# Optimization experiments

Hardware: AMD Instinct MI355X
Metric: run time of the kernel (lower is better)

## Reference

```python
import jax, jax.numpy as jnp
import numpy as np

B, L, D = 64, 1024, 1024


def _attn(q, K, V, mask):
    # q: [B,D], K/V: [B,L,D], mask: [B,L] bool (True = valid)
    scores = jnp.einsum('bd,bld->bl', q, K) / jnp.sqrt(jnp.asarray(D, q.dtype))
    scores = jnp.where(mask, scores, -jnp.inf)
    attn = jax.nn.softmax(scores, axis=-1)
    attn = jnp.where(jnp.isnan(attn), 0.0, attn)  # torch.nan_to_num for all-masked rows
    return jnp.einsum('bl,bld->bd', attn, V)


def setup_inputs() -> dict:
    key = jax.random.key(0)
    ks = jax.random.split(key, 12)
    xav = float(np.sqrt(6.0 / (D + D)))  # xavier_uniform for square Linear
    img_mask = jax.random.randint(ks[4], (B, L), 0, 2).astype(bool)
    txt_mask = jax.random.randint(ks[7], (B, L), 0, 2).astype(bool)
    # guarantee at least one valid token per row
    img_mask = img_mask.at[:, 0].set(True)
    txt_mask = txt_mask.at[:, 0].set(True)
    return {
        'img_q': jax.random.normal(ks[0], (B, D), jnp.float32),
        'txt_q': jax.random.normal(ks[1], (B, D), jnp.float32),
        'K_img': jax.random.normal(ks[2], (B, L, D), jnp.float32),
        'V_img': jax.random.normal(ks[3], (B, L, D), jnp.float32),
        'img_mask': img_mask,
        'K_txt': jax.random.normal(ks[5], (B, L, D), jnp.float32),
        'V_txt': jax.random.normal(ks[6], (B, L, D), jnp.float32),
        'txt_mask': txt_mask,
        'W_img': jax.random.uniform(ks[8], (D, D), jnp.float32, -xav, xav),
        'b_img': jnp.zeros((D,), jnp.float32),
        'W_txt': jax.random.uniform(ks[9], (D, D), jnp.float32, -xav, xav),
        'b_txt': jnp.zeros((D,), jnp.float32),
    }


def reference(img_q, txt_q, K_img, V_img, img_mask, K_txt, V_txt, txt_mask,
              W_img, b_img, W_txt, b_txt):
    # Dropout is identity in eval mode.
    ctx_img = _attn(txt_q, K_img, V_img, img_mask)
    img_q = img_q + ctx_img @ W_img.T + b_img
    ctx_txt = _attn(img_q, K_txt, V_txt, txt_mask)
    txt_q = txt_q + ctx_txt @ W_txt.T + b_txt
    return (img_q, txt_q)
```

## Files before the change

### kernel.cpp

```cpp
#include <hip/hip_runtime.h>
#include <hip/hip_bf16.h>
#include <float.h>

#define B_ 64
#define L_ 1024
#define D_ 1024
#define NSPLIT 8
#define CHUNK 128
#define PSTRIDE 1028

typedef __bf16 bf16x8 __attribute__((ext_vector_type(8)));
typedef float f32x4 __attribute__((ext_vector_type(4)));

__device__ inline unsigned short f2bf(float x) {
    unsigned int u = __float_as_uint(x);
    unsigned int lsb = (u >> 16) & 1u;
    u += 0x7fffu + lsb;
    return (unsigned short)(u >> 16);
}

__global__ __launch_bounds__(512, 2) void attn_kernel(
    const float* __restrict__ q,
    const float* __restrict__ K,
    const float* __restrict__ V,
    const int*   __restrict__ mask,
    float* __restrict__ part,
    const float* __restrict__ cs0,
    const float* __restrict__ cs1,
    unsigned short* __restrict__ cd0,
    unsigned short* __restrict__ cd1,
    int nattn)
{
    const int tid = threadIdx.x;

    if ((int)blockIdx.x >= nattn) {
        int i = ((int)blockIdx.x - nattn) * 512 + tid;
        float4 v0 = reinterpret_cast<const float4*>(cs0)[i];
        float4 v1 = reinterpret_cast<const float4*>(cs1)[i];
        ushort4 u0, u1;
        u0.x = f2bf(v0.x); u0.y = f2bf(v0.y); u0.z = f2bf(v0.z); u0.w = f2bf(v0.w);
        u1.x = f2bf(v1.x); u1.y = f2bf(v1.y); u1.z = f2bf(v1.z); u1.w = f2bf(v1.w);
        reinterpret_cast<ushort4*>(cd0)[i] = u0;
        reinterpret_cast<ushort4*>(cd1)[i] = u1;
        return;
    }

    const int bid  = blockIdx.x;
    const int b    = bid >> 3;
    const int sp   = bid & 7;
    const int l0   = sp * CHUNK;
    const int wave = tid >> 6;
    const int lane = tid & 63;

    __shared__ int   vidx[CHUNK];
    __shared__ float sc[CHUNK];
    __shared__ float pw[CHUNK];
    __shared__ int   nvalid;

    const float4* qptr = reinterpret_cast<const float4*>(q + (size_t)b * D_);
    float4 qreg[4];
    #pragma unroll
    for (int rep = 0; rep < 4; ++rep) qreg[rep] = qptr[lane + rep * 64];

    if (wave == 0) {
        const int* mp = mask + (size_t)b * L_ + l0;
        int mv0 = mp[lane];
        int mv1 = mp[64 + lane];
        unsigned long long bal0 = __ballot(mv0 != 0);
        unsigned long long bal1 = __ballot(mv1 != 0);
        int n0 = __popcll(bal0);
        int nv = n0 + __popcll(bal1);
        unsigned long long lt = (1ull << lane) - 1;
        if (mv0) vidx[__popcll(bal0 & lt)] = lane;
        if (mv1) vidx[n0 + __popcll(bal1 & lt)] = 64 + lane;
        int padv = bal0 ? (__ffsll((long long)bal0) - 1)
                        : (bal1 ? 64 + __ffsll((long long)bal1) - 1 : 0);
        if (nv + lane < CHUNK) vidx[nv + lane] = padv;
        if (lane == 0) nvalid = nv;
    }
    __syncthreads();
    const int nv    = nvalid;
    const int nvp8  = (nv + 7)  & ~7;
    const int nvp16 = (nv + 15) & ~15;

    const float* Kb = K + ((size_t)b * L_ + l0) * D_;
    for (int jj = wave; jj < nvp16; jj += 16) {
        int j2 = jj + 8;
        const float4* k0 = reinterpret_cast<const float4*>(Kb + vidx[jj] * D_);
        const float4* k1 = reinterpret_cast<const float4*>(Kb + vidx[j2] * D_);
        float4 kv0[4], kv1[4];
        #pragma unroll
        for (int rep = 0; rep < 4; ++rep) { kv0[rep] = k0[lane + rep * 64];
                                            kv1[rep] = k1[lane + rep * 64]; }
        float a0a = 0.f, a0b = 0.f, a1a = 0.f, a1b = 0.f;
        #pragma unroll
        for (int rep = 0; rep < 4; rep += 2) {
            a0a += kv0[rep].x * qreg[rep].x + kv0[rep].y * qreg[rep].y
                 + kv0[rep].z * qreg[rep].z + kv0[rep].w * qreg[rep].w;
            a0b += kv0[rep+1].x * qreg[rep+1].x + kv0[rep+1].y * qreg[rep+1].y
                 + kv0[rep+1].z * qreg[rep+1].z + kv0[rep+1].w * qreg[rep+1].w;
            a1a += kv1[rep].x * qreg[rep].x + kv1[rep].y * qreg[rep].y
                 + kv1[rep].z * qreg[rep].z + kv1[rep].w * qreg[rep].w;
            a1b += kv1[rep+1].x * qreg[rep+1].x + kv1[rep+1].y * qreg[rep+1].y
                 + kv1[rep+1].z * qreg[rep+1].z + kv1[rep+1].w * qreg[rep+1].w;
        }
        float a0 = a0a + a0b, a1 = a1a + a1b;
        #pragma unroll
        for (int off = 32; off > 0; off >>= 1) {
            a0 += __shfl_xor(a0, off, 64);
            a1 += __shfl_xor(a1, off, 64);
        }
        if (lane == 0) { sc[jj] = a0 * 0.03125f; sc[j2] = a1 * 0.03125f; }
    }
    __syncthreads();

    if (tid < CHUNK) pw[tid] = (tid < nv) ? __expf(sc[tid]) : 0.f;
    __syncthreads();

    float se = 0.f, ax = 0.f, ay = 0.f;
    const float2* vbase = reinterpret_cast<const float2*>(V + ((size_t)b * L_ + l0) * D_);
    for (int j = 0; j < nvp8; j += 8) {
        float p[8]; int ix[8];
        #pragma unroll
        for (int t = 0; t < 8; ++t) { p[t] = pw[j + t]; ix[t] = vidx[j + t]; }
        float2 vv[8];
        #pragma unroll
        for (int t = 0; t < 8; ++t) vv[t] = vbase[ix[t] * (D_ / 2) + tid];
        #pragma unroll
        for (int t = 0; t < 8; ++t) {
            se += p[t];
            ax += p[t] * vv[t].x; ay += p[t] * vv[t].y;
        }
    }

    float* po = part + (size_t)bid * PSTRIDE;
    float2 o; o.x = ax; o.y = ay;
    reinterpret_cast<float2*>(po)[tid] = o;
    if (tid == 0) po[D_] = se;
}

__global__ __launch_bounds__(256) void proj_kernel(
    const float* __restrict__ part,
    const unsigned short* __restrict__ Wbf,
    const float* __restrict__ qin,
    const float* __restrict__ bias,
    float* __restrict__ out)
{
    const int tid  = threadIdx.x;
    const int wave = tid >> 6;
    const int lane = tid & 63;
    const int m0   = (blockIdx.x & 3) * 16;
    const int n0   = (blockIdx.x >> 2) * 16;
    const int r    = lane & 15;
    const int g    = lane >> 4;

    __shared__ float invd[16];
    if (tid < 128) {
        int rr = tid >> 3, s = tid & 7;
        float se = part[((size_t)(m0 + rr) * 8 + s) * PSTRIDE + D_];
        se += __shfl_xor(se, 1, 64);
        se += __shfl_xor(se, 2, 64);
        se += __shfl_xor(se, 4, 64);
        if (s == 0) invd[rr] = 1.f / se;
    }
    __syncthreads();
    const float inv = invd[r];

    const float* pa = part + ((size_t)(m0 + r) * 8) * PSTRIDE + wave * 256 + g * 8;
    const bf16x8* bptr = reinterpret_cast<const bf16x8*>(
        Wbf + (size_t)(n0 + r) * D_ + g * 8 + wave * 256);

    f32x4 acc = {0.f, 0.f, 0.f, 0.f};
    #pragma unroll
    for (int kk = 0; kk < 8; ++kk) {
        float a[8] = {0.f,0.f,0.f,0.f,0.f,0.f,0.f,0.f};
        #pragma unroll
        for (int s = 0; s < 8; ++s) {
            float4 p0 = *reinterpret_cast<const float4*>(pa + s * PSTRIDE + kk * 32);
            float4 p1 = *reinterpret_cast<const float4*>(pa + s * PSTRIDE + kk * 32 + 4);
            a[0] += p0.x; a[1] += p0.y; a[2] += p0.z; a[3] += p0.w;
            a[4] += p1.x; a[5] += p1.y; a[6] += p1.z; a[7] += p1.w;
        }
        bf16x8 av;
        #pragma unroll
        for (int j = 0; j < 8; ++j) av[j] = (__bf16)(a[j] * inv);
        bf16x8 bb = bptr[kk * 4];
        acc = __builtin_amdgcn_mfma_f32_16x16x32_bf16(av, bb, acc, 0, 0, 0);
    }

    __shared__ float red[1024];
    #pragma unroll
    for (int i = 0; i < 4; ++i) red[wave * 256 + lane * 4 + i] = acc[i];
    __syncthreads();

    int ol = tid >> 2, oi = tid & 3;
    float v = red[ol * 4 + oi] + red[256 + ol * 4 + oi]
            + red[512 + ol * 4 + oi] + red[768 + ol * 4 + oi];
    int row = m0 + ((ol >> 4) * 4 + oi);
    int col = n0 + (ol & 15);
    out[(size_t)row * D_ + col] = qin[(size_t)row * D_ + col] + bias[col] + v;
}

extern "C" void kernel_launch(void* const* d_in, const int* in_sizes, int n_in,
                              void* d_out, int out_size, void* d_ws, size_t ws_size,
                              hipStream_t stream) {
    const float* img_q    = (const float*)d_in[0];
    const float* txt_q    = (const float*)d_in[1];
    const float* K_img    = (const float*)d_in[2];
    const float* V_img    = (const float*)d_in[3];
    const int*   img_mask = (const int*)  d_in[4];
    const float* K_txt    = (const float*)d_in[5];
    const float* V_txt    = (const float*)d_in[6];
    const int*   txt_mask = (const int*)  d_in[7];
    const float* W_img    = (const float*)d_in[8];
    const float* b_img    = (const float*)d_in[9];
    const float* W_txt    = (const float*)d_in[10];
    const float* b_txt    = (const float*)d_in[11];

    float* out_img = (float*)d_out;
    float* out_txt = (float*)d_out + B_ * D_;

    char* ws = (char*)d_ws;
    float* part = (float*)ws;
    size_t part_bytes = (size_t)B_ * NSPLIT * PSTRIDE * sizeof(float);
    unsigned short* Wimg_bf = (unsigned short*)(ws + part_bytes);
    unsigned short* Wtxt_bf = Wimg_bf + (size_t)D_ * D_;

    attn_kernel<<<1024, 512, 0, stream>>>(
        txt_q, K_img, V_img, img_mask, part,
        W_img, W_txt, Wimg_bf, Wtxt_bf, B_ * NSPLIT);
    proj_kernel<<<256, 256, 0, stream>>>(part, Wimg_bf, img_q, b_img, out_img);
    attn_kernel<<<512, 512, 0, stream>>>(
        out_img, K_txt, V_txt, txt_mask, part,
        nullptr, nullptr, nullptr, nullptr, B_ * NSPLIT);
    proj_kernel<<<256, 256, 0, stream>>>(part, Wtxt_bf, txt_q, b_txt, out_txt);
}
```

Baseline: 152.3 us.

## Reduce split partials once per row tile in proj; widen V loads to float4

The projection kernel changes from 256 small blocks to 32 blocks of 512 threads. Each block sums the 8 split partials for its 16 rows once, scales them by the softmax denominator, stores them as bf16 in LDS, and then has 8 waves each compute 16 output columns over the full K. Before, every 16x16 output tile re-read and re-summed the partials, so the new layout removes that redundant traffic. The cost is far fewer blocks and a longer serial chain of MFMA steps per wave. In the attention kernel, the P·V loop now uses float4 loads, with the two halves of the block taking alternating groups of 8 rows, followed by an LDS reduction between the halves.

```diff
diff --git a/kernel.cpp b/kernel.cpp
--- a/kernel.cpp
+++ b/kernel.cpp
@@ -52,10 +52,12 @@
     const int wave = tid >> 6;
     const int lane = tid & 63;
 
-    __shared__ int   vidx[CHUNK];
-    __shared__ float sc[CHUNK];
-    __shared__ float pw[CHUNK];
-    __shared__ int   nvalid;
+    __shared__ int    vidx[CHUNK];
+    __shared__ float  sc[CHUNK];
+    __shared__ float  pw[CHUNK];
+    __shared__ float4 red4[512];
+    __shared__ float  seb[2];
+    __shared__ int    nvalid;
 
     const float4* qptr = reinterpret_cast<const float4*>(q + (size_t)b * D_);
     float4 qreg[4];
@@ -80,7 +82,6 @@
     }
     __syncthreads();
     const int nv    = nvalid;
-    const int nvp8  = (nv + 7)  & ~7;
     const int nvp16 = (nv + 15) & ~15;
 
     const float* Kb = K + ((size_t)b * L_ + l0) * D_;
@@ -117,29 +118,40 @@
     if (tid < CHUNK) pw[tid] = (tid < nv) ? __expf(sc[tid]) : 0.f;
     __syncthreads();
 
-    float se = 0.f, ax = 0.f, ay = 0.f;
-    const float2* vbase = reinterpret_cast<const float2*>(V + ((size_t)b * L_ + l0) * D_);
-    for (int j = 0; j < nvp8; j += 8) {
+    const int half = tid >> 8;
+    const int dsl  = tid & 255;
+    float se = 0.f, ax = 0.f, ay = 0.f, az = 0.f, aw = 0.f;
+    const float4* vb = reinterpret_cast<const float4*>(V + ((size_t)b * L_ + l0) * D_);
+    for (int j = 0; j < nvp16; j += 16) {
+        int base = j + half * 8;
         float p[8]; int ix[8];
         #pragma unroll
-        for (int t = 0; t < 8; ++t) { p[t] = pw[j + t]; ix[t] = vidx[j + t]; }
-        float2 vv[8];
-        #pragma unroll
-        for (int t = 0; t < 8; ++t) vv[t] = vbase[ix[t] * (D_ / 2) + tid];
+        for (int t = 0; t < 8; ++t) { p[t] = pw[base + t]; ix[t] = vidx[base + t]; }
+        float4 vv[8];
+        #pragma unroll
+        for (int t = 0; t < 8; ++t) vv[t] = vb[ix[t] * (D_ / 4) + dsl];
         #pragma unroll
         for (int t = 0; t < 8; ++t) {
             se += p[t];
             ax += p[t] * vv[t].x; ay += p[t] * vv[t].y;
-        }
-    }
+            az += p[t] * vv[t].z; aw += p[t] * vv[t].w;
+        }
+    }
+    float4 o4; o4.x = ax; o4.y = ay; o4.z = az; o4.w = aw;
+    red4[tid] = o4;
+    if (dsl == 0) seb[half] = se;
+    __syncthreads();
 
     float* po = part + (size_t)bid * PSTRIDE;
-    float2 o; o.x = ax; o.y = ay;
-    reinterpret_cast<float2*>(po)[tid] = o;
-    if (tid == 0) po[D_] = se;
-}
-
-__global__ __launch_bounds__(256) void proj_kernel(
+    if (tid < 256) {
+        float4 a = red4[tid], c = red4[tid + 256];
+        float4 o; o.x = a.x + c.x; o.y = a.y + c.y; o.z = a.z + c.z; o.w = a.w + c.w;
+        reinterpret_cast<float4*>(po)[tid] = o;
+    }
+    if (tid == 0) po[D_] = seb[0] + seb[1];
+}
+
+__global__ __launch_bounds__(512) void proj_kernel(
     const float* __restrict__ part,
     const unsigned short* __restrict__ Wbf,
     const float* __restrict__ qin,
@@ -147,14 +159,14 @@
     float* __restrict__ out)
 {
     const int tid  = threadIdx.x;
+    const int m0   = (blockIdx.x >> 3) * 16;
+    const int ns   = blockIdx.x & 7;
     const int wave = tid >> 6;
     const int lane = tid & 63;
-    const int m0   = (blockIdx.x & 3) * 16;
-    const int n0   = (blockIdx.x >> 2) * 16;
-    const int r    = lane & 15;
-    const int g    = lane >> 4;
-
-    __shared__ float invd[16];
+
+    __shared__ float  invd[16];
+    __shared__ __bf16 A_lds[128 * 16 * 8];
+
     if (tid < 128) {
         int rr = tid >> 3, s = tid & 7;
         float se = part[((size_t)(m0 + rr) * 8 + s) * PSTRIDE + D_];
@@ -164,41 +176,53 @@
         if (s == 0) invd[rr] = 1.f / se;
     }
     __syncthreads();
-    const float inv = invd[r];
-
-    const float* pa = part + ((size_t)(m0 + r) * 8) * PSTRIDE + wave * 256 + g * 8;
+
+    {
+        int r  = tid >> 5;
+        int k0 = (tid & 31) * 32;
+        const float* pb = part + ((size_t)(m0 + r) * 8) * PSTRIDE + k0;
+        float a[32];
+        #pragma unroll
+        for (int i = 0; i < 32; ++i) a[i] = 0.f;
+        #pragma unroll
+        for (int s = 0; s < 8; ++s) {
+            #pragma unroll
+            for (int g = 0; g < 8; ++g) {
+                float4 v = *reinterpret_cast<const float4*>(pb + s * PSTRIDE + g * 4);
+                a[g*4+0] += v.x; a[g*4+1] += v.y; a[g*4+2] += v.z; a[g*4+3] += v.w;
+            }
+        }
+        float inv = invd[r];
+        #pragma unroll
+        for (int gg = 0; gg < 4; ++gg) {
+            bf16x8 w;
+            #pragma unroll
+            for (int j = 0; j < 8; ++j) w[j] = (__bf16)(a[gg*8+j] * inv);
+            *reinterpret_cast<bf16x8*>(&A_lds[(((k0 >> 3) + gg) * 16 + r) * 8]) = w;
+        }
+    }
+    __syncthreads();
+
+    const int n0 = ns * 128 + wave * 16;
+    const int r  = lane & 15;
+    const int g  = lane >> 4;
     const bf16x8* bptr = reinterpret_cast<const bf16x8*>(
-        Wbf + (size_t)(n0 + r) * D_ + g * 8 + wave * 256);
+        Wbf + (size_t)(n0 + r) * D_ + g * 8);
 
     f32x4 acc = {0.f, 0.f, 0.f, 0.f};
     #pragma unroll
-    for (int kk = 0; kk < 8; ++kk) {
-        float a[8] = {0.f,0.f,0.f,0.f,0.f,0.f,0.f,0.f};
-        #pragma unroll
-        for (int s = 0; s < 8; ++s) {
-            float4 p0 = *reinterpret_cast<const float4*>(pa + s * PSTRIDE + kk * 32);
-            float4 p1 = *reinterpret_cast<const float4*>(pa + s * PSTRIDE + kk * 32 + 4);
-            a[0] += p0.x; a[1] += p0.y; a[2] += p0.z; a[3] += p0.w;
-            a[4] += p1.x; a[5] += p1.y; a[6] += p1.z; a[7] += p1.w;
-        }
-        bf16x8 av;
-        #pragma unroll
-        for (int j = 0; j < 8; ++j) av[j] = (__bf16)(a[j] * inv);
+    for (int kk = 0; kk < 32; ++kk) {
+        bf16x8 a  = *reinterpret_cast<const bf16x8*>(&A_lds[((kk*4 + g) * 16 + r) * 8]);
         bf16x8 bb = bptr[kk * 4];
-        acc = __builtin_amdgcn_mfma_f32_16x16x32_bf16(av, bb, acc, 0, 0, 0);
-    }
-
-    __shared__ float red[1024];
+        acc = __builtin_amdgcn_mfma_f32_16x16x32_bf16(a, bb, acc, 0, 0, 0);
+    }
+
+    int col  = n0 + r;
+    int row0 = m0 + g * 4;
     #pragma unroll
-    for (int i = 0; i < 4; ++i) red[wave * 256 + lane * 4 + i] = acc[i];
-    __syncthreads();
-
-    int ol = tid >> 2, oi = tid & 3;
-    float v = red[ol * 4 + oi] + red[256 + ol * 4 + oi]
-            + red[512 + ol * 4 + oi] + red[768 + ol * 4 + oi];
-    int row = m0 + ((ol >> 4) * 4 + oi);
-    int col = n0 + (ol & 15);
-    out[(size_t)row * D_ + col] = qin[(size_t)row * D_ + col] + bias[col] + v;
+    for (int j = 0; j < 4; ++j)
+        out[(size_t)(row0 + j) * D_ + col] =
+            qin[(size_t)(row0 + j) * D_ + col] + bias[col] + acc[j];
 }
 
 extern "C" void kernel_launch(void* const* d_in, const int* in_sizes, int n_in,
@@ -229,9 +253,9 @@
     attn_kernel<<<1024, 512, 0, stream>>>(
         txt_q, K_img, V_img, img_mask, part,
         W_img, W_txt, Wimg_bf, Wtxt_bf, B_ * NSPLIT);
-    proj_kernel<<<256, 256, 0, stream>>>(part, Wimg_bf, img_q, b_img, out_img);
+    proj_kernel<<<32, 512, 0, stream>>>(part, Wimg_bf, img_q, b_img, out_img);
     attn_kernel<<<512, 512, 0, stream>>>(
         out_img, K_txt, V_txt, txt_mask, part,
         nullptr, nullptr, nullptr, nullptr, B_ * NSPLIT);
-    proj_kernel<<<256, 256, 0, stream>>>(part, Wtxt_bf, txt_q, b_txt, out_txt);
-}
+    proj_kernel<<<32, 512, 0, stream>>>(part, Wtxt_bf, txt_q, b_txt, out_txt);
+}
```

Result: slower. 163.7 us (+7.5%).
